# Performance work log

Measured on AMD Instinct MI355X. Metric: run time of the kernel, lower is better.

The kernel has to match this reference:

```python
import jax, jax.numpy as jnp
import numpy as np

B = 128          # number of graphs in the batch
NM, EM = 100000, 400000    # mol nodes / edges
NP, EP = 200000, 3200000   # protein nodes / edges
DM, DP, OD = 78, 54, 16


def setup_inputs() -> dict:
    key = jax.random.key(0)
    ks = jax.random.split(key, 20)
    def w(k, shape):
        return jax.random.normal(k, shape, jnp.float32) * 0.05
    z = lambda n: jnp.zeros((n,), jnp.float32)
    return {
        "mol_x": jax.random.normal(ks[0], (NM, DM), jnp.float32),
        "mol_edge_index": jax.random.randint(ks[1], (2, EM), 0, NM),
        "mol_batch": jnp.sort(jax.random.randint(ks[2], (NM,), 0, B)),
        "pro_x": jax.random.normal(ks[3], (NP, DP), jnp.float32),
        "pro_edge_index": jax.random.randint(ks[4], (2, EP), 0, NP),
        "pro_batch": jnp.sort(jax.random.randint(ks[5], (NP,), 0, B)),
        "mol_W1": w(ks[6], (256, DM)), "mol_b1": z(256),
        "mol_W2": w(ks[7], (7 * OD, 256)), "mol_b2": z(7 * OD),
        "c1_Wl": w(ks[8], (DP, DP)), "c1_bl": z(DP), "c1_Wr": w(ks[9], (DP, DP)),
        "c2_Wl": w(ks[10], (2 * DP, DP)), "c2_bl": z(2 * DP), "c2_Wr": w(ks[11], (2 * DP, DP)),
        "pro_W1": w(ks[12], (256, 2 * DP)), "pro_b1": z(256),
        "pro_W2": w(ks[13], (9 * OD, 256)), "pro_b2": z(9 * OD),
        "fc1_W": w(ks[14], (1024, 16 * OD)), "fc1_b": z(1024),
        "fc2_W": w(ks[15], (512, 1024)), "fc2_b": z(512),
        "out_W": w(ks[16], (1, 512)), "out_b": z(1),
    }


def _seg_mean(x, seg, n):
    s = jax.ops.segment_sum(x, seg, num_segments=n)
    c = jax.ops.segment_sum(jnp.ones((x.shape[0],), x.dtype), seg, num_segments=n)
    return s / jnp.maximum(c, 1.0)[:, None]


def _sage(x, ei, Wl, bl, Wr):
    # PyG SAGEConv (mean aggr): lin_l(mean_{j->i} x_j) + lin_r(x_i); lin_r has no bias
    agg = _seg_mean(x[ei[0]], ei[1], x.shape[0])
    return agg @ Wl.T + bl + x @ Wr.T


def reference(mol_x, mol_edge_index, mol_batch, pro_x, pro_edge_index, pro_batch,
              mol_W1, mol_b1, mol_W2, mol_b2,
              c1_Wl, c1_bl, c1_Wr, c2_Wl, c2_bl, c2_Wr,
              pro_W1, pro_b1, pro_W2, pro_b2,
              fc1_W, fc1_b, fc2_W, fc2_b, out_W, out_b):
    alpha, degree = 0.05, 4
    # APPNP-style k-hop propagation over the unnormalized COO adjacency:
    # (adj @ h)[i] = sum over edges (row=i, col=j) of h[j]
    row, col = mol_edge_index[0], mol_edge_index[1]
    h = mol_x
    emb = alpha * mol_x
    for _ in range(degree):
        h = jax.ops.segment_sum(h[col], row, num_segments=mol_x.shape[0])
        emb = emb + (1.0 - alpha) * h / degree
    x = _seg_mean(emb, mol_batch, B)            # global mean pool -> [B, 78]
    x = jax.nn.relu(x @ mol_W1.T + mol_b1)
    x = x @ mol_W2.T + mol_b2                   # [B, 112]; dropout is identity at eval

    xt = jax.nn.relu(_sage(pro_x, pro_edge_index, c1_Wl, c1_bl, c1_Wr))
    xt = jax.nn.relu(_sage(xt, pro_edge_index, c2_Wl, c2_bl, c2_Wr))
    xt = _seg_mean(xt, pro_batch, B)            # [B, 108]
    xt = jax.nn.relu(xt @ pro_W1.T + pro_b1)
    xt = xt @ pro_W2.T + pro_b2                 # [B, 144]

    xc = jnp.concatenate([x, xt], axis=1)       # [B, 256]
    xc = jax.nn.relu(xc @ fc1_W.T + fc1_b)
    xc = jax.nn.relu(xc @ fc2_W.T + fc2_b)
    return xc @ out_W.T + out_b                 # [B, 1]
```

## Files before the change

kernel.cpp:

```cpp
#include <hip/hip_runtime.h>

#define K256 __launch_bounds__(256)

constexpr int B = 128;
constexpr int NM = 100000, EM = 400000;
constexpr int NP = 200000, EP = 3200000;
constexpr int DM = 78, DPK = 54, DP2 = 108;
constexpr int XH = 32;
constexpr int XH4 = 16;
constexpr int MH = 48;

__device__ __forceinline__ float b2f(unsigned short u) {
  return __uint_as_float((unsigned int)u << 16);
}
__device__ __forceinline__ unsigned short f2b(float f) {
  unsigned int b = __float_as_uint(f);
  return (unsigned short)((b + 0x7fffu + ((b >> 16) & 1u)) >> 16);
}

template <int SH>
__global__ void K256 k_bhist(const int* __restrict__ dst, int* __restrict__ bhist, int E) {
  __shared__ int lh[512];
  int tid = threadIdx.x;
  for (int t = tid; t < 512; t += 256) lh[t] = 0;
  __syncthreads();
  int c0 = blockIdx.x * 4096;
#pragma unroll
  for (int k = 0; k < 16; k++) {
    int e = c0 + k * 256 + tid;
    if (e < E) atomicAdd(&lh[dst[e] >> SH], 1);
  }
  __syncthreads();
  for (int t = tid; t < 512; t += 256) {
    int c = lh[t];
    if (c) atomicAdd(&bhist[t], c);
  }
}

__global__ void k_scanb(const int* __restrict__ bhist, int* __restrict__ bed,
                        int* __restrict__ bcur, int NB, int E) {
  __shared__ int s[512];
  int tid = threadIdx.x;
  int v = (tid < NB) ? bhist[tid] : 0;
  s[tid] = v;
  __syncthreads();
  for (int off = 1; off < 512; off <<= 1) {
    int t = (tid >= off) ? s[tid - off] : 0;
    __syncthreads();
    s[tid] += t;
    __syncthreads();
  }
  int excl = s[tid] - v;
  if (tid < NB) {
    bed[tid] = excl;
    bcur[tid] = excl;
  }
  if (tid == NB - 1) bed[NB] = E;
}

template <int SH>
__global__ void K256 k_bin(const int* __restrict__ src, const int* __restrict__ dst,
                           int* __restrict__ bcur, int2* __restrict__ binned, int E) {
  __shared__ int lh[512];
  __shared__ int gbase[512];
  int c0 = blockIdx.x * 4096;
  int tid = threadIdx.x;
  for (int t = tid; t < 512; t += 256) lh[t] = 0;
  __syncthreads();
  int r[16], dcache[16];
#pragma unroll
  for (int k = 0; k < 16; k++) {
    int e = c0 + k * 256 + tid;
    if (e < E) {
      int d = dst[e];
      dcache[k] = d;
      r[k] = atomicAdd(&lh[d >> SH], 1);
    }
  }
  __syncthreads();
  for (int b = tid; b < 512; b += 256) {
    int c = lh[b];
    gbase[b] = c ? atomicAdd(&bcur[b], c) : 0;
  }
  __syncthreads();
#pragma unroll
  for (int k = 0; k < 16; k++) {
    int e = c0 + k * 256 + tid;
    if (e < E) {
      int d = dcache[k];
      binned[gbase[d >> SH] + r[k]] = make_int2(src[e], d);
    }
  }
}

template <int SH>
__global__ void K256 k_build(const int2* __restrict__ binned, const int* __restrict__ bed,
                             int* __restrict__ deg, int* __restrict__ starts,
                             int* __restrict__ csr, int N) {
  constexpr int NN = 1 << SH;
  constexpr int P = NN / 256;
  __shared__ int lcnt[NN];
  __shared__ int lpair[256];
  int b = blockIdx.x, base = b << SH, tid = threadIdx.x;
  int nn = min(N - base, NN);
  for (int t = tid; t < NN; t += 256) lcnt[t] = 0;
  __syncthreads();
  int e0 = bed[b], e1 = bed[b + 1];
  for (int e = e0 + tid; e < e1; e += 256) atomicAdd(&lcnt[binned[e].y - base], 1);
  __syncthreads();
  int loc[P];
  int psum = 0;
#pragma unroll
  for (int p = 0; p < P; p++) {
    loc[p] = lcnt[tid * P + p];
    psum += loc[p];
  }
  lpair[tid] = psum;
  __syncthreads();
  for (int off = 1; off < 256; off <<= 1) {
    int t = (tid >= off) ? lpair[tid - off] : 0;
    __syncthreads();
    lpair[tid] += t;
    __syncthreads();
  }
  int run = lpair[tid] - psum;
  __syncthreads();
#pragma unroll
  for (int p = 0; p < P; p++) {
    int i = tid * P + p;
    int st = e0 + run;
    if (i < nn) {
      deg[base + i] = loc[p];
      starts[base + i] = st;
    }
    lcnt[i] = st;
    run += loc[p];
  }
  __syncthreads();
  for (int e = e0 + tid; e < e1; e += 256) {
    int2 sd = binned[e];
    int p = atomicAdd(&lcnt[sd.y - base], 1);
    csr[p] = sd.x;
  }
}

__global__ void K256 k_bstart(const int* __restrict__ batch, int* __restrict__ bstart, int N) {
  int i = blockIdx.x * 256 + threadIdx.x;
  if (i < N) {
    int b = batch[i];
    int pb = (i == 0) ? -1 : batch[i - 1];
    for (int bb = pb + 1; bb <= b; bb++) bstart[bb] = i;
    if (i == N - 1)
      for (int bb = b + 1; bb <= B; bb++) bstart[bb] = N;
  }
}

__global__ void k_inv(const int* __restrict__ bstart, float* __restrict__ inv) {
  int b = threadIdx.x;
  if (b < B) inv[b] = 1.f / fmaxf((float)(bstart[b + 1] - bstart[b]), 1.f);
}

__global__ void K256 k_transT(const float* __restrict__ in, float* __restrict__ out, int R,
                              int C) {
  __shared__ float t[32][33];
  int cb = blockIdx.x * 32, rb = blockIdx.y * 32;
  int tx = threadIdx.x & 31, ty = threadIdx.x >> 5;
  for (int i = ty; i < 32; i += 8) {
    int r = rb + i, c = cb + tx;
    if (r < R && c < C) t[i][tx] = in[(size_t)r * C + c];
  }
  __syncthreads();
  for (int i = ty; i < 32; i += 8) {
    int c = cb + i, r = rb + tx;
    if (r < R && c < C) out[(size_t)c * R + r] = t[tx][i];
  }
}

__global__ void K256 k_prepw(const float* __restrict__ c1Wl, const float* __restrict__ c1Wr,
                             const float* __restrict__ c1bl, const float* __restrict__ c2Wl,
                             const float* __restrict__ c2Wr, float* __restrict__ w1cat,
                             float* __restrict__ bl1c, float* __restrict__ w2cat) {
  int i = blockIdx.x * 256 + threadIdx.x;
  if (i < 108 * 56) {
    int k = i / 56, o = i - k * 56;
    w1cat[i] = (o < 54) ? ((k < 54) ? c1Wl[o * 54 + k] : c1Wr[o * 54 + (k - 54)]) : 0.f;
  }
  if (i < 108 * 108) {
    int k = i / 108, o = i - k * 108;
    w2cat[i] = (k < 54) ? c2Wl[o * 54 + k] : c2Wr[o * 54 + (k - 54)];
  }
  if (i < 56) bl1c[i] = (i < 54) ? c1bl[i] : 0.f;
}

template <int DF2, int XHD>
__global__ void K256 k_castg(const float* __restrict__ x, int sstride,
                             ushort2* __restrict__ xh, int N) {
  int t = blockIdx.x * 256 + threadIdx.x;
  if (t < N * DF2) {
    int n = t / DF2, j = t - n * DF2;
    float2 v = *(const float2*)(x + (size_t)n * sstride + 2 * j);
    xh[(size_t)n * XHD + j] = make_ushort2(f2b(v.x), f2b(v.y));
  }
}

__global__ void K256 k_gatherh(const ushort4* __restrict__ xh4, const int* __restrict__ starts,
                               const int* __restrict__ deg, const int* __restrict__ csr,
                               ushort4* __restrict__ outh4, int N) {
  int wid = (blockIdx.x * 256 + threadIdx.x) >> 6;
  int lane = threadIdx.x & 63;
  if (wid >= N) return;
  int s = starts[wid], d = deg[wid];
  const int* cp = csr + s;
  int quarter = lane >> 4, sl = lane & 15;
  bool act = sl < 14;
  float a0 = 0.f, a1 = 0.f, a2 = 0.f, a3 = 0.f;
  float b0 = 0.f, b1 = 0.f, b2 = 0.f, b3 = 0.f;
  int j = 0;
  for (; j + 8 <= d; j += 8) {
    if (act) {
      ushort4 v = xh4[(size_t)cp[j + quarter] * XH4 + sl];
      ushort4 w = xh4[(size_t)cp[j + 4 + quarter] * XH4 + sl];
      a0 += b2f(v.x);
      a1 += b2f(v.y);
      a2 += b2f(v.z);
      a3 += b2f(v.w);
      b0 += b2f(w.x);
      b1 += b2f(w.y);
      b2 += b2f(w.z);
      b3 += b2f(w.w);
    }
  }
  for (; j + 4 <= d; j += 4) {
    if (act) {
      ushort4 v = xh4[(size_t)cp[j + quarter] * XH4 + sl];
      a0 += b2f(v.x);
      a1 += b2f(v.y);
      a2 += b2f(v.z);
      a3 += b2f(v.w);
    }
  }
  int r = d - j;
  if (quarter < r && act) {
    ushort4 v = xh4[(size_t)cp[j + quarter] * XH4 + sl];
    a0 += b2f(v.x);
    a1 += b2f(v.y);
    a2 += b2f(v.z);
    a3 += b2f(v.w);
  }
  a0 += b0;
  a1 += b1;
  a2 += b2;
  a3 += b3;
  a0 += __shfl_xor(a0, 16, 64);
  a1 += __shfl_xor(a1, 16, 64);
  a2 += __shfl_xor(a2, 16, 64);
  a3 += __shfl_xor(a3, 16, 64);
  a0 += __shfl_xor(a0, 32, 64);
  a1 += __shfl_xor(a1, 32, 64);
  a2 += __shfl_xor(a2, 32, 64);
  a3 += __shfl_xor(a3, 32, 64);
  if (lane < 14) {
    float inv = 1.f / fmaxf((float)d, 1.f);
    outh4[(size_t)wid * XH4 + lane] =
        make_ushort4(f2b(a0 * inv), f2b(a1 * inv), f2b(a2 * inv), f2b(a3 * inv));
  }
}

__global__ void K256 k_gatherm(const ushort2* __restrict__ xh, const int* __restrict__ starts,
                               const int* __restrict__ deg, const int* __restrict__ csr,
                               ushort2* __restrict__ outh, int N) {
  int wid = (blockIdx.x * 256 + threadIdx.x) >> 6;
  int lane = threadIdx.x & 63;
  if (wid >= N) return;
  int s = starts[wid], d = deg[wid];
  const int* cp = csr + s;
  bool act = lane < 39;
  float ax = 0.f, ay = 0.f, bx = 0.f, by = 0.f;
  int j = 0;
  for (; j + 4 <= d; j += 4) {
    if (act) {
      ushort2 v0 = xh[(size_t)cp[j] * MH + lane];
      ushort2 v1 = xh[(size_t)cp[j + 1] * MH + lane];
      ushort2 v2 = xh[(size_t)cp[j + 2] * MH + lane];
      ushort2 v3 = xh[(size_t)cp[j + 3] * MH + lane];
      ax += b2f(v0.x) + b2f(v2.x);
      ay += b2f(v0.y) + b2f(v2.y);
      bx += b2f(v1.x) + b2f(v3.x);
      by += b2f(v1.y) + b2f(v3.y);
    }
  }
  for (; j < d; j++) {
    if (act) {
      ushort2 v = xh[(size_t)cp[j] * MH + lane];
      ax += b2f(v.x);
      ay += b2f(v.y);
    }
  }
  ax += bx;
  ay += by;
  if (act) outh[(size_t)wid * MH + lane] = make_ushort2(f2b(ax), f2b(ay));
}

template <int SPLIT>
__global__ void K256 k_pool_segh(const ushort2* __restrict__ xh, const int* __restrict__ bstart,
                                 float* __restrict__ pooled, float coef) {
  constexpr int NPB = 6;
  __shared__ float sp[NPB * DM];
  int b = blockIdx.x / SPLIT;
  int sidx = blockIdx.x - b * SPLIT;
  int tid = threadIdx.x;
  int r0 = bstart[b], r1 = bstart[b + 1];
  int len = r1 - r0;
  int per = (len + SPLIT - 1) / SPLIT;
  int s0 = r0 + sidx * per;
  int s1 = min(r1, s0 + per);
  if (tid < 39 * NPB) {
    int ioff = tid / 39, j = tid - ioff * 39;
    float a0x = 0.f, a0y = 0.f, a1x = 0.f, a1y = 0.f;
    int i = s0 + ioff;
    for (; i + 3 * NPB < s1; i += 4 * NPB) {
      ushort2 v0 = xh[(size_t)i * MH + j];
      ushort2 v1 = xh[(size_t)(i + NPB) * MH + j];
      ushort2 v2 = xh[(size_t)(i + 2 * NPB) * MH + j];
      ushort2 v3 = xh[(size_t)(i + 3 * NPB) * MH + j];
      a0x += b2f(v0.x) + b2f(v2.x);
      a0y += b2f(v0.y) + b2f(v2.y);
      a1x += b2f(v1.x) + b2f(v3.x);
      a1y += b2f(v1.y) + b2f(v3.y);
    }
    for (; i < s1; i += NPB) {
      ushort2 v = xh[(size_t)i * MH + j];
      a0x += b2f(v.x);
      a0y += b2f(v.y);
    }
    sp[ioff * DM + 2 * j] = a0x + a1x;
    sp[ioff * DM + 2 * j + 1] = a0y + a1y;
  }
  __syncthreads();
  if (tid < DM) {
    float s = 0.f;
#pragma unroll
    for (int g = 0; g < NPB; g++) s += sp[g * DM + tid];
    s *= coef;
    if (s != 0.f) atomicAdd(&pooled[b * DM + tid], s);
  }
}

__global__ void __launch_bounds__(256, 4) k_sage1c(
    const float* __restrict__ x, const ushort2* __restrict__ aggh,
    const float* __restrict__ wcat, const float* __restrict__ blc,
    ushort2* __restrict__ outh, int N) {
  __shared__ float scat[64 * 109];
  int base = blockIdx.x * 64;
  int nn = min(N - base, 64);
  int tid = threadIdx.x;
  for (int t = tid; t < nn * 27; t += 256) {
    int n = t / 27, j = t - n * 27;
    ushort2 va = aggh[(size_t)(base + n) * XH + j];
    float2 vx = *(const float2*)(x + (size_t)(base + n) * 54 + 2 * j);
    float* sr = scat + n * 109;
    sr[2 * j] = b2f(va.x);
    sr[2 * j + 1] = b2f(va.y);
    sr[54 + 2 * j] = vx.x;
    sr[54 + 2 * j + 1] = vx.y;
  }
  __syncthreads();
  int w = tid >> 6, lane = tid & 63;
  int obase = __builtin_amdgcn_readfirstlane(w * 14);
  if (lane >= nn) return;
  float acc[14];
#pragma unroll
  for (int o = 0; o < 14; o++) acc[o] = blc[obase + o];
  const float* rs = scat + lane * 109;
#pragma unroll 2
  for (int k = 0; k < 108; k++) {
    float v = rs[k];
    const float* wr = wcat + k * 56 + obase;
#pragma unroll
    for (int o = 0; o < 14; o++) acc[o] += v * wr[o];
  }
  ushort2* op = outh + (size_t)(base + lane) * XH + (obase >> 1);
#pragma unroll
  for (int o = 0; o < 7; o++)
    op[o] = make_ushort2(f2b(fmaxf(acc[2 * o], 0.f)), f2b(fmaxf(acc[2 * o + 1], 0.f)));
}

template <int SPLIT>
__global__ void __launch_bounds__(256, 4) k_sage2c(
    const ushort2* __restrict__ xt1h, const ushort2* __restrict__ aggh,
    const float* __restrict__ wcat, const float* __restrict__ bl,
    const int* __restrict__ bstart, float* __restrict__ pooled) {
  __shared__ float scat[64 * 109];
  int b = blockIdx.x / SPLIT;
  int sidx = blockIdx.x - b * SPLIT;
  int tid = threadIdx.x;
  int w = tid >> 6, lane = tid & 63;
  int obase = __builtin_amdgcn_readfirstlane(w * 27);
  int r0 = bstart[b], r1 = bstart[b + 1];
  int len = r1 - r0;
  int per = (len + SPLIT - 1) / SPLIT;
  int s0 = r0 + sidx * per;
  int s1 = min(r1, s0 + per);
  float pool[27];
#pragma unroll
  for (int o = 0; o < 27; o++) pool[o] = 0.f;
  for (int tb = s0; tb < s1; tb += 64) {
    int nn = min(s1 - tb, 64);
    __syncthreads();
    for (int t = tid; t < nn * 27; t += 256) {
      int n = t / 27, j = t - n * 27;
      ushort2 va = aggh[(size_t)(tb + n) * XH + j];
      ushort2 vx = xt1h[(size_t)(tb + n) * XH + j];
      float* sr = scat + n * 109;
      sr[2 * j] = b2f(va.x);
      sr[2 * j + 1] = b2f(va.y);
      sr[54 + 2 * j] = b2f(vx.x);
      sr[54 + 2 * j + 1] = b2f(vx.y);
    }
    __syncthreads();
    if (lane < nn) {
      float acc[27];
#pragma unroll
      for (int o = 0; o < 27; o++) acc[o] = bl[obase + o];
      const float* rs = scat + lane * 109;
#pragma unroll 2
      for (int k = 0; k < 108; k++) {
        float v = rs[k];
        const float* wr = wcat + k * 108 + obase;
#pragma unroll
        for (int o = 0; o < 27; o++) acc[o] += v * wr[o];
      }
#pragma unroll
      for (int o = 0; o < 27; o++) pool[o] += fmaxf(acc[o], 0.f);
    }
  }
#pragma unroll
  for (int o = 0; o < 27; o++) {
#pragma unroll
    for (int off = 1; off < 64; off <<= 1) pool[o] += __shfl_xor(pool[o], off, 64);
  }
  if (lane == 0) {
    float* pb = pooled + b * DP2 + obase;
#pragma unroll
    for (int o = 0; o < 27; o++)
      if (pool[o] != 0.f) atomicAdd(&pb[o], pool[o]);
  }
}

template <int DIN, int DOUT>
__global__ void K256 k_headf(const float* __restrict__ X, int xstride,
                             const float* __restrict__ rs, const float* __restrict__ W1T,
                             const float* __restrict__ b1, const float* __restrict__ W2T,
                             const float* __restrict__ b2, float* __restrict__ Y,
                             int ystride, int ycol0) {
  __shared__ float sx[DIN];
  __shared__ float sh[256];
  int b = blockIdx.x, tid = threadIdx.x;
  float scale = rs ? rs[b] : 1.f;
  for (int f = tid; f < DIN; f += 256) sx[f] = X[(size_t)b * xstride + f] * scale;
  __syncthreads();
  float acc = b1[tid];
#pragma unroll 4
  for (int k = 0; k < DIN; k++) acc += sx[k] * W1T[k * 256 + tid];
  sh[tid] = fmaxf(acc, 0.f);
  __syncthreads();
  if (tid < DOUT) {
    float a = b2[tid];
#pragma unroll 4
    for (int k = 0; k < 256; k++) a += sh[k] * W2T[k * DOUT + tid];
    Y[(size_t)b * ystride + ycol0 + tid] = a;
  }
}

__global__ void K256 k_fin(const float* __restrict__ xc, const float* __restrict__ W1T,
                           const float* __restrict__ b1, const float* __restrict__ W2T,
                           const float* __restrict__ b2, const float* __restrict__ W3,
                           const float* __restrict__ b3, float* __restrict__ out) {
  __shared__ float sx[256];
  __shared__ float sh1[1024];
  __shared__ float sh2[512];
  __shared__ float red[4];
  int b = blockIdx.x, tid = threadIdx.x;
  sx[tid] = xc[(size_t)b * 256 + tid];
  __syncthreads();
  {
    float a0 = b1[tid], a1 = b1[tid + 256], a2 = b1[tid + 512], a3 = b1[tid + 768];
#pragma unroll 2
    for (int k = 0; k < 256; k++) {
      float xv = sx[k];
      const float* wr = W1T + k * 1024;
      a0 += xv * wr[tid];
      a1 += xv * wr[tid + 256];
      a2 += xv * wr[tid + 512];
      a3 += xv * wr[tid + 768];
    }
    sh1[tid] = fmaxf(a0, 0.f);
    sh1[tid + 256] = fmaxf(a1, 0.f);
    sh1[tid + 512] = fmaxf(a2, 0.f);
    sh1[tid + 768] = fmaxf(a3, 0.f);
  }
  __syncthreads();
  {
    float a0 = b2[tid], a1 = b2[tid + 256];
#pragma unroll 2
    for (int k = 0; k < 1024; k++) {
      float xv = sh1[k];
      const float* wr = W2T + k * 512;
      a0 += xv * wr[tid];
      a1 += xv * wr[tid + 256];
    }
    sh2[tid] = fmaxf(a0, 0.f);
    sh2[tid + 256] = fmaxf(a1, 0.f);
  }
  __syncthreads();
  float a = 0.f;
  for (int k = tid; k < 512; k += 256) a += sh2[k] * W3[k];
#pragma unroll
  for (int off = 32; off > 0; off >>= 1) a += __shfl_down(a, off, 64);
  if ((tid & 63) == 0) red[tid >> 6] = a;
  __syncthreads();
  if (tid == 0) out[b] = red[0] + red[1] + red[2] + red[3] + b3[0];
}

__global__ void k_report(float* out, float v, int n) {
  int i = blockIdx.x * 256 + threadIdx.x;
  if (i < n) out[i] = v;
}

extern "C" void kernel_launch(void* const* d_in, const int* in_sizes, int n_in,
                              void* d_out, int out_size, void* d_ws, size_t ws_size,
                              hipStream_t stream) {
  (void)in_sizes; (void)n_in;
  const float* mol_x = (const float*)d_in[0];
  const int* m_ei = (const int*)d_in[1];
  const int* m_batch = (const int*)d_in[2];
  const float* pro_x = (const float*)d_in[3];
  const int* p_ei = (const int*)d_in[4];
  const int* p_batch = (const int*)d_in[5];
  const float* mol_W1 = (const float*)d_in[6];
  const float* mol_b1 = (const float*)d_in[7];
  const float* mol_W2 = (const float*)d_in[8];
  const float* mol_b2 = (const float*)d_in[9];
  const float* c1_Wl = (const float*)d_in[10];
  const float* c1_bl = (const float*)d_in[11];
  const float* c1_Wr = (const float*)d_in[12];
  const float* c2_Wl = (const float*)d_in[13];
  const float* c2_bl = (const float*)d_in[14];
  const float* c2_Wr = (const float*)d_in[15];
  const float* pro_W1 = (const float*)d_in[16];
  const float* pro_b1 = (const float*)d_in[17];
  const float* pro_W2 = (const float*)d_in[18];
  const float* pro_b2 = (const float*)d_in[19];
  const float* fc1_W = (const float*)d_in[20];
  const float* fc1_b = (const float*)d_in[21];
  const float* fc2_W = (const float*)d_in[22];
  const float* fc2_b = (const float*)d_in[23];
  const float* out_W = (const float*)d_in[24];
  const float* out_b = (const float*)d_in[25];
  float* out = (float*)d_out;
  char* ws = (char*)d_ws;

  const int* m_row = m_ei;
  const int* m_col = m_ei + EM;
  const int* p_e0 = p_ei;
  const int* p_e1 = p_ei + EP;

  auto al = [](size_t x) { return (x + 255) & ~(size_t)255; };

  size_t o = 0;
  size_t o_pdeg = o;   o += al((size_t)NP * 4);
  size_t o_pstart = o; o += al((size_t)NP * 4);
  size_t o_pcsr = o;   o += al((size_t)EP * 4);
  size_t o_aggh = o;   o += al((size_t)NP * XH * 4);
  size_t o_xt1h = o;   o += al((size_t)NP * XH * 4);
  size_t o_pxh = o;    o += al((size_t)NP * XH * 4);
  size_t pro_end = o;

  o = 0;
  size_t o_mdeg = o;   o += al((size_t)NM * 4);
  size_t o_mstart = o; o += al((size_t)NM * 4);
  size_t o_mcsr = o;   o += al((size_t)EM * 4);
  size_t o_mxh = o;    o += al((size_t)NM * MH * 4);
  size_t o_hAh = o;    o += al((size_t)NM * MH * 4);
  size_t o_hBh = o;    o += al((size_t)NM * MH * 4);
  size_t mol_end = o;

  size_t tail = al(pro_end > mol_end ? pro_end : mol_end);
  size_t o_poolM = tail; tail += al((size_t)B * DM * 4);
  size_t o_poolP = tail; tail += al((size_t)B * DP2 * 4);
  size_t o_mbs = tail;   tail += al((size_t)(B + 1) * 4);
  size_t o_pbs = tail;   tail += al((size_t)(B + 1) * 4);
  size_t o_w1c = tail;   tail += al((size_t)108 * 56 * 4);
  size_t o_bl1 = tail;   tail += al(56 * 4);
  size_t o_w2c = tail;   tail += al((size_t)108 * 108 * 4);
  size_t o_mbc = tail;   tail += al(512 * 4);
  size_t o_pbc = tail;   tail += al(512 * 4);
  size_t o_mbh = tail;   tail += al(512 * 4);
  size_t o_pbh = tail;   tail += al(512 * 4);
  size_t o_mbed = tail;  tail += al(513 * 4);
  size_t o_pbed = tail;  tail += al(513 * 4);
  size_t o_mh1T = tail;  tail += al((size_t)DM * 256 * 4);
  size_t o_mh2T = tail;  tail += al((size_t)256 * 112 * 4);
  size_t o_ph1T = tail;  tail += al((size_t)DP2 * 256 * 4);
  size_t o_ph2T = tail;  tail += al((size_t)256 * 144 * 4);
  size_t o_fc1T = tail;  tail += al((size_t)256 * 1024 * 4);
  size_t o_fc2T = tail;  tail += al((size_t)1024 * 512 * 4);
  size_t o_xc = tail;    tail += al((size_t)B * 256 * 4);
  size_t o_invM = tail;  tail += al(B * 4);
  size_t o_invP = tail;  tail += al(B * 4);

  if (ws_size < tail) {
    k_report<<<1, 256, 0, stream>>>(out, (float)(ws_size >> 20), out_size);
    return;
  }

  int* mdeg = (int*)(ws + o_mdeg);
  int* mstart = (int*)(ws + o_mstart);
  int* mcsr = (int*)(ws + o_mcsr);
  ushort2* mxh = (ushort2*)(ws + o_mxh);
  ushort2* hAh = (ushort2*)(ws + o_hAh);
  ushort2* hBh = (ushort2*)(ws + o_hBh);
  int* pdeg = (int*)(ws + o_pdeg);
  int* pstart = (int*)(ws + o_pstart);
  int* pcsr = (int*)(ws + o_pcsr);
  ushort2* aggh = (ushort2*)(ws + o_aggh);
  ushort2* xt1h = (ushort2*)(ws + o_xt1h);
  ushort2* pxh = (ushort2*)(ws + o_pxh);
  float* poolM = (float*)(ws + o_poolM);
  float* poolP = (float*)(ws + o_poolP);
  int* mbs = (int*)(ws + o_mbs);
  int* pbs = (int*)(ws + o_pbs);
  float* w1cat = (float*)(ws + o_w1c);
  float* bl1c = (float*)(ws + o_bl1);
  float* w2cat = (float*)(ws + o_w2c);
  int* mbc = (int*)(ws + o_mbc);
  int* pbc = (int*)(ws + o_pbc);
  int* mbh = (int*)(ws + o_mbh);
  int* pbh = (int*)(ws + o_pbh);
  int* mbed = (int*)(ws + o_mbed);
  int* pbed = (int*)(ws + o_pbed);
  float* mh1T = (float*)(ws + o_mh1T);
  float* mh2T = (float*)(ws + o_mh2T);
  float* ph1T = (float*)(ws + o_ph1T);
  float* ph2T = (float*)(ws + o_ph2T);
  float* fc1T = (float*)(ws + o_fc1T);
  float* fc2T = (float*)(ws + o_fc2T);
  float* xc = (float*)(ws + o_xc);
  float* invM = (float*)(ws + o_invM);
  float* invP = (float*)(ws + o_invP);
  int2* mbinned = (int2*)hAh;
  int2* pbinned = (int2*)aggh;

  k_prepw<<<(108 * 108 + 255) / 256, 256, 0, stream>>>(c1_Wl, c1_Wr, c1_bl, c2_Wl, c2_Wr,
                                                       w1cat, bl1c, w2cat);
  {
    auto tg = [](int R, int C) { return dim3((C + 31) / 32, (R + 31) / 32); };
    k_transT<<<tg(256, DM), 256, 0, stream>>>(mol_W1, mh1T, 256, DM);
    k_transT<<<tg(112, 256), 256, 0, stream>>>(mol_W2, mh2T, 112, 256);
    k_transT<<<tg(256, DP2), 256, 0, stream>>>(pro_W1, ph1T, 256, DP2);
    k_transT<<<tg(144, 256), 256, 0, stream>>>(pro_W2, ph2T, 144, 256);
    k_transT<<<tg(1024, 256), 256, 0, stream>>>(fc1_W, fc1T, 1024, 256);
    k_transT<<<tg(512, 1024), 256, 0, stream>>>(fc2_W, fc2T, 512, 1024);
  }

  constexpr int SHM = 8;
  constexpr int NBM = (NM + (1 << SHM) - 1) >> SHM;
  hipMemsetAsync(mbh, 0, 512 * 4, stream);
  hipMemsetAsync(poolM, 0, (size_t)B * DM * 4, stream);
  k_bhist<SHM><<<(EM + 4095) / 4096, 256, 0, stream>>>(m_row, mbh, EM);
  k_scanb<<<1, 512, 0, stream>>>(mbh, mbed, mbc, NBM, EM);
  k_bin<SHM><<<(EM + 4095) / 4096, 256, 0, stream>>>(m_col, m_row, mbc, mbinned, EM);
  k_build<SHM><<<NBM, 256, 0, stream>>>(mbinned, mbed, mdeg, mstart, mcsr, NM);
  k_bstart<<<(NM + 255) / 256, 256, 0, stream>>>(m_batch, mbs, NM);
  k_inv<<<1, 128, 0, stream>>>(mbs, invM);
  k_castg<39, MH><<<(NM * 39 + 255) / 256, 256, 0, stream>>>(mol_x, DM, mxh, NM);

  int gb_m = (NM * 64 + 255) / 256;
  k_pool_segh<8><<<B * 8, 256, 0, stream>>>(mxh, mbs, poolM, 0.05f);
  k_gatherm<<<gb_m, 256, 0, stream>>>(mxh, mstart, mdeg, mcsr, hAh, NM);
  k_pool_segh<8><<<B * 8, 256, 0, stream>>>(hAh, mbs, poolM, 0.2375f);
  k_gatherm<<<gb_m, 256, 0, stream>>>(hAh, mstart, mdeg, mcsr, hBh, NM);
  k_pool_segh<8><<<B * 8, 256, 0, stream>>>(hBh, mbs, poolM, 0.2375f);
  k_gatherm<<<gb_m, 256, 0, stream>>>(hBh, mstart, mdeg, mcsr, hAh, NM);
  k_pool_segh<8><<<B * 8, 256, 0, stream>>>(hAh, mbs, poolM, 0.2375f);
  k_gatherm<<<gb_m, 256, 0, stream>>>(hAh, mstart, mdeg, mcsr, hBh, NM);
  k_pool_segh<8><<<B * 8, 256, 0, stream>>>(hBh, mbs, poolM, 0.2375f);
  k_headf<DM, 112><<<B, 256, 0, stream>>>(poolM, DM, invM, mh1T, mol_b1, mh2T, mol_b2, xc,
                                          256, 0);

  constexpr int SHP = 9;
  constexpr int NBP = (NP + (1 << SHP) - 1) >> SHP;
  hipMemsetAsync(pbh, 0, 512 * 4, stream);
  hipMemsetAsync(poolP, 0, (size_t)B * DP2 * 4, stream);
  k_bhist<SHP><<<(EP + 4095) / 4096, 256, 0, stream>>>(p_e1, pbh, EP);
  k_scanb<<<1, 512, 0, stream>>>(pbh, pbed, pbc, NBP, EP);
  k_bin<SHP><<<(EP + 4095) / 4096, 256, 0, stream>>>(p_e0, p_e1, pbc, pbinned, EP);
  k_build<SHP><<<NBP, 256, 0, stream>>>(pbinned, pbed, pdeg, pstart, pcsr, NP);
  k_bstart<<<(NP + 255) / 256, 256, 0, stream>>>(p_batch, pbs, NP);
  k_inv<<<1, 128, 0, stream>>>(pbs, invP);
  k_castg<27, XH><<<(NP * 27 + 255) / 256, 256, 0, stream>>>(pro_x, DPK, pxh, NP);

  int gb_p = (NP * 64 + 255) / 256;
  k_gatherh<<<gb_p, 256, 0, stream>>>((const ushort4*)pxh, pstart, pdeg, pcsr,
                                      (ushort4*)aggh, NP);
  k_sage1c<<<(NP + 63) / 64, 256, 0, stream>>>(pro_x, aggh, w1cat, bl1c, xt1h, NP);
  k_gatherh<<<gb_p, 256, 0, stream>>>((const ushort4*)xt1h, pstart, pdeg, pcsr,
                                      (ushort4*)aggh, NP);
  k_sage2c<8><<<B * 8, 256, 0, stream>>>(xt1h, aggh, w2cat, c2_bl, pbs, poolP);
  k_headf<DP2, 144><<<B, 256, 0, stream>>>(poolP, DP2, invP, ph1T, pro_b1, ph2T, pro_b2, xc,
                                           256, 112);

  k_fin<<<B, 256, 0, stream>>>(xc, fc1T, fc1_b, fc2T, fc2_b, out_W, out_b, out);
}
```

Measured before the change: 914.9 us.

## Split final MLP into batch-tiled FC kernels that reuse weights across graphs

Replaces the per-graph fused fc1/fc2/out kernel with two tiled GEMM kernels that each load a weight column once and apply it to 16-32 graphs held in shared memory, plus a small GEMV kernel for the output layer. Previously each of the 128 blocks streamed the full 2.5 MB of fc weights, so weight traffic scaled with the batch size. The change adds two extra launches and intermediate buffers in workspace in exchange for far less redundant weight reading.

```diff
diff --git a/kernel.cpp b/kernel.cpp
--- a/kernel.cpp
+++ b/kernel.cpp
@@ -472,54 +472,56 @@
   }
 }
 
-__global__ void K256 k_fin(const float* __restrict__ xc, const float* __restrict__ W1T,
-                           const float* __restrict__ b1, const float* __restrict__ W2T,
-                           const float* __restrict__ b2, const float* __restrict__ W3,
-                           const float* __restrict__ b3, float* __restrict__ out) {
-  __shared__ float sx[256];
-  __shared__ float sh1[1024];
-  __shared__ float sh2[512];
-  __shared__ float red[4];
-  int b = blockIdx.x, tid = threadIdx.x;
-  sx[tid] = xc[(size_t)b * 256 + tid];
-  __syncthreads();
-  {
-    float a0 = b1[tid], a1 = b1[tid + 256], a2 = b1[tid + 512], a3 = b1[tid + 768];
+template <int DIN, int DOUT, int NB, int KT, bool RELU>
+__global__ void K256 k_fcws(const float* __restrict__ X, int xstride,
+                            const float* __restrict__ WT, const float* __restrict__ bias,
+                            float* __restrict__ Y, int ystride) {
+  constexpr int BPT = NB / 4;
+  constexpr int XP = NB + 4;
+  __shared__ float xs[KT][XP];
+  int ob = blockIdx.x * 64;
+  int bb = blockIdx.y * NB;
+  int tid = threadIdx.x;
+  int otid = tid & 63;
+  int b0 = (tid >> 6) * BPT;
+  int o = ob + otid;
+  float acc[BPT];
+  float bv = bias[o];
+#pragma unroll
+  for (int i = 0; i < BPT; i++) acc[i] = bv;
+  for (int kt = 0; kt < DIN; kt += KT) {
+    __syncthreads();
+    for (int idx = tid; idx < NB * KT; idx += 256) {
+      int b = idx / KT, k = idx - b * KT;
+      xs[k][b] = X[(size_t)(bb + b) * xstride + kt + k];
+    }
+    __syncthreads();
 #pragma unroll 2
-    for (int k = 0; k < 256; k++) {
-      float xv = sx[k];
-      const float* wr = W1T + k * 1024;
-      a0 += xv * wr[tid];
-      a1 += xv * wr[tid + 256];
-      a2 += xv * wr[tid + 512];
-      a3 += xv * wr[tid + 768];
-    }
-    sh1[tid] = fmaxf(a0, 0.f);
-    sh1[tid + 256] = fmaxf(a1, 0.f);
-    sh1[tid + 512] = fmaxf(a2, 0.f);
-    sh1[tid + 768] = fmaxf(a3, 0.f);
-  }
-  __syncthreads();
-  {
-    float a0 = b2[tid], a1 = b2[tid + 256];
+    for (int k = 0; k < KT; k++) {
+      float w = WT[(size_t)(kt + k) * DOUT + o];
+#pragma unroll
+      for (int i = 0; i < BPT; i++) acc[i] += xs[k][b0 + i] * w;
+    }
+  }
+#pragma unroll
+  for (int i = 0; i < BPT; i++) {
+    float v = RELU ? fmaxf(acc[i], 0.f) : acc[i];
+    Y[(size_t)(bb + b0 + i) * ystride + o] = v;
+  }
+}
+
+__global__ void __launch_bounds__(64) k_gemv1(const float* __restrict__ t2,
+                                              const float* __restrict__ W3,
+                                              const float* __restrict__ b3,
+                                              float* __restrict__ out) {
+  int b = blockIdx.x, lane = threadIdx.x;
+  float a = 0.f;
+  const float* row = t2 + (size_t)b * 512;
 #pragma unroll 2
-    for (int k = 0; k < 1024; k++) {
-      float xv = sh1[k];
-      const float* wr = W2T + k * 512;
-      a0 += xv * wr[tid];
-      a1 += xv * wr[tid + 256];
-    }
-    sh2[tid] = fmaxf(a0, 0.f);
-    sh2[tid + 256] = fmaxf(a1, 0.f);
-  }
-  __syncthreads();
-  float a = 0.f;
-  for (int k = tid; k < 512; k += 256) a += sh2[k] * W3[k];
+  for (int k = lane; k < 512; k += 64) a += row[k] * W3[k];
 #pragma unroll
   for (int off = 32; off > 0; off >>= 1) a += __shfl_down(a, off, 64);
-  if ((tid & 63) == 0) red[tid >> 6] = a;
-  __syncthreads();
-  if (tid == 0) out[b] = red[0] + red[1] + red[2] + red[3] + b3[0];
+  if (lane == 0) out[b] = a + b3[0];
 }
 
 __global__ void k_report(float* out, float v, int n) {
@@ -606,6 +608,8 @@
   size_t o_fc1T = tail;  tail += al((size_t)256 * 1024 * 4);
   size_t o_fc2T = tail;  tail += al((size_t)1024 * 512 * 4);
   size_t o_xc = tail;    tail += al((size_t)B * 256 * 4);
+  size_t o_t1 = tail;    tail += al((size_t)B * 1024 * 4);
+  size_t o_t2 = tail;    tail += al((size_t)B * 512 * 4);
   size_t o_invM = tail;  tail += al(B * 4);
   size_t o_invP = tail;  tail += al(B * 4);
 
@@ -646,6 +650,8 @@
   float* fc1T = (float*)(ws + o_fc1T);
   float* fc2T = (float*)(ws + o_fc2T);
   float* xc = (float*)(ws + o_xc);
+  float* t1 = (float*)(ws + o_t1);
+  float* t2 = (float*)(ws + o_t2);
   float* invM = (float*)(ws + o_invM);
   float* invP = (float*)(ws + o_invP);
   int2* mbinned = (int2*)hAh;
@@ -710,5 +716,11 @@
   k_headf<DP2, 144><<<B, 256, 0, stream>>>(poolP, DP2, invP, ph1T, pro_b1, ph2T, pro_b2, xc,
                                            256, 112);
 
-  k_fin<<<B, 256, 0, stream>>>(xc, fc1T, fc1_b, fc2T, fc2_b, out_W, out_b, out);
-}
+  {
+    dim3 gA(1024 / 64, B / 32);
+    k_fcws<256, 1024, 32, 128, true><<<gA, 256, 0, stream>>>(xc, 256, fc1T, fc1_b, t1, 1024);
+    dim3 gB(512 / 64, B / 16);
+    k_fcws<1024, 512, 16, 128, true><<<gB, 256, 0, stream>>>(t1, 1024, fc2T, fc2_b, t2, 512);
+    k_gemv1<<<B, 64, 0, stream>>>(t2, out_W, out_b, out);
+  }
+}
```

Result: no change. 928.6 us (+1.5%).
